# Performance work log

Measured on AMD Instinct MI355X. Metric: run time of the kernel, lower is better.

The kernel has to match this reference:

```python
import jax, jax.numpy as jnp
import numpy as np

EMB = 128
WIN = 5
OUT = 128
VOCAB = 50257
PAD_IDX = 0


def setup_inputs() -> dict:
    key = jax.random.key(0)
    k1, k2, k3 = jax.random.split(key, 3)
    x = jax.random.randint(k1, (16, 2048), 0, VOCAB, dtype=jnp.int64 if jax.config.jax_enable_x64 else jnp.int32)
    emb_table = jax.random.normal(k2, (VOCAB, EMB), dtype=jnp.float32)
    emb_table = emb_table.at[PAD_IDX].set(0.0)  # padding_idx row is zero
    fan_in = EMB * WIN
    bound = 1.0 / np.sqrt(fan_in)
    kw, kb = jax.random.split(k3)
    W = jax.random.uniform(kw, (OUT, fan_in), minval=-bound, maxval=bound, dtype=jnp.float32)
    b = jax.random.uniform(kb, (OUT,), minval=-bound, maxval=bound, dtype=jnp.float32)
    return {"x": x, "emb_table": emb_table, "W": W, "b": b}


def reference(x, emb_table, W, b):
    B, S = x.shape
    no_pads = (WIN - 1) // 2
    emb = emb_table[x]                                   # (B, S, EMB) gather
    padded = jnp.pad(emb, ((0, 0), (no_pads, no_pads), (0, 0)))
    windows = jnp.stack([padded[:, k:k + S] for k in range(WIN)], axis=2)
    flat = windows.reshape(B, S, WIN * EMB)
    y = jnp.einsum('bsk,ok->bso', flat, W) + b           # (B, S, OUT)
    return jax.nn.gelu(y, approximate=False)             # torch GELU default is exact
```

## Files before the change

### kernel.cpp

```cpp
#include <hip/hip_runtime.h>
#include <hip/hip_bf16.h>


#define EMB   128
#define WIN   5
#define OUTC  128
#define SEQ   2048
#define KTOT  640
#define MTILE 64
#define NTILE 64

#define EMB_STRIDE 136
#define SW_STRIDE  136

typedef __bf16  bf16x8 __attribute__((ext_vector_type(8)));
typedef float   f32x4  __attribute__((ext_vector_type(4)));
typedef ushort  u16x8  __attribute__((ext_vector_type(8)));

__device__ inline ushort f2bf(float f) {
    __bf16 h = (__bf16)f;
    return __builtin_bit_cast(ushort, h);
}

__device__ inline u16x8 cvt8v(float4 v0, float4 v1) {
    u16x8 o;
    o[0] = f2bf(v0.x); o[1] = f2bf(v0.y); o[2] = f2bf(v0.z); o[3] = f2bf(v0.w);
    o[4] = f2bf(v1.x); o[5] = f2bf(v1.y); o[6] = f2bf(v1.z); o[7] = f2bf(v1.w);
    return o;
}

__global__ __launch_bounds__(256, 4) void conv_encoder_kernel(
    const int* __restrict__ x,
    const float* __restrict__ emb,
    const float* __restrict__ W,
    const float* __restrict__ bias,
    float* __restrict__ out)
{
    __shared__ ushort sEmb[(MTILE + WIN - 1) * EMB_STRIDE];
    __shared__ ushort sW[NTILE * SW_STRIDE];

    const int tid = threadIdx.x;
    const int mi  = blockIdx.x;
    const int n0  = blockIdx.y * NTILE;
    const int m0  = mi * MTILE;
    const int bb  = m0 >> 11;
    const int s0  = m0 & (SEQ - 1);

    float4 preA[4], preB[4];
    #pragma unroll
    for (int t = 0; t < 4; ++t) {
        const int idx = tid + t * 256;
        const int r = idx >> 4, c = idx & 15;
        const float* p = W + (size_t)(n0 + r) * KTOT + c * 8;
        preA[t] = *(const float4*)p;
        preB[t] = *(const float4*)(p + 4);
    }

    {
        const int xbase = bb * SEQ;
        for (int idx = tid; idx < (MTILE + WIN - 1) * 16; idx += 256) {
            const int r = idx >> 4, c = idx & 15;
            const int s = s0 - 2 + r;
            const int tok = (s >= 0 && s < SEQ) ? x[xbase + s] : 0;
            const float* p = emb + (size_t)tok * EMB + c * 8;
            *(u16x8*)(&sEmb[r * EMB_STRIDE + c * 8]) =
                cvt8v(*(const float4*)p, *(const float4*)(p + 4));
        }
    }

    const int lane = tid & 63;
    const int wv   = tid >> 6;
    const int qr   = (wv >> 1) * 32;
    const int qc   = (wv & 1) * 32;
    const int lr   = lane & 15;
    const int lk8  = (lane >> 4) * 8;

    f32x4 acc[2][2];
    #pragma unroll
    for (int i = 0; i < 2; ++i)
        #pragma unroll
        for (int j = 0; j < 2; ++j)
            acc[i][j] = (f32x4){0.f, 0.f, 0.f, 0.f};

    for (int win = 0; win < WIN; ++win) {
        __syncthreads();
        #pragma unroll
        for (int t = 0; t < 4; ++t) {
            const int idx = tid + t * 256;
            const int r = idx >> 4, c = idx & 15;
            *(u16x8*)(&sW[r * SW_STRIDE + c * 8]) = cvt8v(preA[t], preB[t]);
        }
        __syncthreads();

        if (win + 1 < WIN) {
            #pragma unroll
            for (int t = 0; t < 4; ++t) {
                const int idx = tid + t * 256;
                const int r = idx >> 4, c = idx & 15;
                const float* p = W + (size_t)(n0 + r) * KTOT + (win + 1) * EMB + c * 8;
                preA[t] = *(const float4*)p;
                preB[t] = *(const float4*)(p + 4);
            }
        }

        #pragma unroll
        for (int kc = 0; kc < 4; ++kc) {
            const int e = kc * 32 + lk8;
            bf16x8 afr[2], bfr[2];
            #pragma unroll
            for (int i = 0; i < 2; ++i)
                afr[i] = *(const bf16x8*)(&sEmb[(qr + i * 16 + lr + win) * EMB_STRIDE + e]);
            #pragma unroll
            for (int j = 0; j < 2; ++j)
                bfr[j] = *(const bf16x8*)(&sW[(qc + j * 16 + lr) * SW_STRIDE + e]);
            #pragma unroll
            for (int i = 0; i < 2; ++i)
                #pragma unroll
                for (int j = 0; j < 2; ++j)
                    acc[i][j] = __builtin_amdgcn_mfma_f32_16x16x32_bf16(afr[i], bfr[j], acc[i][j], 0, 0, 0);
        }
    }

    float bj[2];
    #pragma unroll
    for (int j = 0; j < 2; ++j)
        bj[j] = bias[n0 + qc + j * 16 + lr];

    const int rbase = (lane >> 4) * 4;
    #pragma unroll
    for (int i = 0; i < 2; ++i) {
        #pragma unroll
        for (int j = 0; j < 2; ++j) {
            const int col = n0 + qc + j * 16 + lr;
            #pragma unroll
            for (int r = 0; r < 4; ++r) {
                const int row = m0 + qr + i * 16 + rbase + r;
                const float y = acc[i][j][r] + bj[j];
                const float g = 0.5f * y * (1.0f + erff(y * 0.70710678118654752f));
                out[(size_t)row * OUTC + col] = g;
            }
        }
    }
}

extern "C" void kernel_launch(void* const* d_in, const int* in_sizes, int n_in,
                              void* d_out, int out_size, void* d_ws, size_t ws_size,
                              hipStream_t stream) {
    (void)in_sizes; (void)n_in; (void)d_ws; (void)ws_size; (void)out_size;
    const int* x        = (const int*)d_in[0];
    const float* emb    = (const float*)d_in[1];
    const float* Wm     = (const float*)d_in[2];
    const float* bias   = (const float*)d_in[3];
    float* out          = (float*)d_out;

    dim3 grid(32768 / MTILE, OUTC / NTILE);
    dim3 block(256);
    hipLaunchKernelGGL(conv_encoder_kernel, grid, block, 0, stream, x, emb, Wm, bias, out);
}
```

Measured before the change: 93.29 us.

## Pre-convert gathered embeddings and weights to bf16 in a separate prep kernel

```diff
diff --git a/kernel.cpp b/kernel.cpp
--- a/kernel.cpp
+++ b/kernel.cpp
@@ -11,7 +11,16 @@
 #define NTILE 64
 
 #define EMB_STRIDE 136
-#define SW_STRIDE  136
+
+#define ABF_OFF   0
+#define ABF_BYTES (32768ull * 128 * 2)
+#define WBF_OFF   ABF_BYTES
+#define WBF_BYTES (128ull * 640 * 2)
+#define ZROW_OFF  (WBF_OFF + WBF_BYTES)
+#define NTASK_A   (32768 * 16)
+#define NTASK_W   (10240)
+#define NTASK_Z   (16)
+#define NTASK_TOT (NTASK_A + NTASK_W + NTASK_Z)
 
 typedef __bf16  bf16x8 __attribute__((ext_vector_type(8)));
 typedef float   f32x4  __attribute__((ext_vector_type(4)));
@@ -29,15 +38,38 @@
     return o;
 }
 
-__global__ __launch_bounds__(256, 4) void conv_encoder_kernel(
+__global__ __launch_bounds__(256) void prep_kernel(
     const int* __restrict__ x,
     const float* __restrict__ emb,
     const float* __restrict__ W,
+    ushort* __restrict__ ws)
+{
+    int t = blockIdx.x * 256 + threadIdx.x;
+    for (; t < NTASK_TOT; t += gridDim.x * 256) {
+        if (t < NTASK_A) {
+            const int row = t >> 4, c = t & 15;
+            const int tok = x[row];
+            const float* p = emb + (size_t)tok * EMB + c * 8;
+            *(u16x8*)(ws + (size_t)row * EMB + c * 8) =
+                cvt8v(*(const float4*)p, *(const float4*)(p + 4));
+        } else if (t < NTASK_A + NTASK_W) {
+            const int i = t - NTASK_A;
+            const float* p = W + (size_t)i * 8;
+            *(u16x8*)(ws + WBF_OFF / 2 + (size_t)i * 8) =
+                cvt8v(*(const float4*)p, *(const float4*)(p + 4));
+        } else {
+            const int i = t - NTASK_A - NTASK_W;
+            *(u16x8*)(ws + ZROW_OFF / 2 + (size_t)i * 8) = (u16x8){0,0,0,0,0,0,0,0};
+        }
+    }
+}
+
+__global__ __launch_bounds__(256, 4) void conv_encoder_kernel(
+    const ushort* __restrict__ ws,
     const float* __restrict__ bias,
     float* __restrict__ out)
 {
     __shared__ ushort sEmb[(MTILE + WIN - 1) * EMB_STRIDE];
-    __shared__ ushort sW[NTILE * SW_STRIDE];
 
     const int tid = threadIdx.x;
     const int mi  = blockIdx.x;
@@ -46,27 +78,19 @@
     const int bb  = m0 >> 11;
     const int s0  = m0 & (SEQ - 1);
 
-    float4 preA[4], preB[4];
-    #pragma unroll
-    for (int t = 0; t < 4; ++t) {
-        const int idx = tid + t * 256;
+    const ushort* Abf  = ws;
+    const ushort* Wbf  = ws + WBF_OFF / 2;
+    const ushort* zrow = ws + ZROW_OFF / 2;
+
+    for (int idx = tid; idx < (MTILE + WIN - 1) * 16; idx += 256) {
         const int r = idx >> 4, c = idx & 15;
-        const float* p = W + (size_t)(n0 + r) * KTOT + c * 8;
-        preA[t] = *(const float4*)p;
-        preB[t] = *(const float4*)(p + 4);
+        const int s = s0 - 2 + r;
+        const ushort* src = (s >= 0 && s < SEQ)
+            ? Abf + ((size_t)(bb * SEQ + s)) * EMB + c * 8
+            : zrow + c * 8;
+        *(u16x8*)(&sEmb[r * EMB_STRIDE + c * 8]) = *(const u16x8*)src;
     }
-
-    {
-        const int xbase = bb * SEQ;
-        for (int idx = tid; idx < (MTILE + WIN - 1) * 16; idx += 256) {
-            const int r = idx >> 4, c = idx & 15;
-            const int s = s0 - 2 + r;
-            const int tok = (s >= 0 && s < SEQ) ? x[xbase + s] : 0;
-            const float* p = emb + (size_t)tok * EMB + c * 8;
-            *(u16x8*)(&sEmb[r * EMB_STRIDE + c * 8]) =
-                cvt8v(*(const float4*)p, *(const float4*)(p + 4));
-        }
-    }
+    __syncthreads();
 
     const int lane = tid & 63;
     const int wv   = tid >> 6;
@@ -82,37 +106,20 @@
         for (int j = 0; j < 2; ++j)
             acc[i][j] = (f32x4){0.f, 0.f, 0.f, 0.f};
 
+    const ushort* wbase0 = Wbf + (size_t)(n0 + qc + lr) * KTOT + lk8;
+    const ushort* wbase1 = wbase0 + 16 * KTOT;
+
     for (int win = 0; win < WIN; ++win) {
-        __syncthreads();
-        #pragma unroll
-        for (int t = 0; t < 4; ++t) {
-            const int idx = tid + t * 256;
-            const int r = idx >> 4, c = idx & 15;
-            *(u16x8*)(&sW[r * SW_STRIDE + c * 8]) = cvt8v(preA[t], preB[t]);
-        }
-        __syncthreads();
-
-        if (win + 1 < WIN) {
-            #pragma unroll
-            for (int t = 0; t < 4; ++t) {
-                const int idx = tid + t * 256;
-                const int r = idx >> 4, c = idx & 15;
-                const float* p = W + (size_t)(n0 + r) * KTOT + (win + 1) * EMB + c * 8;
-                preA[t] = *(const float4*)p;
-                preB[t] = *(const float4*)(p + 4);
-            }
-        }
-
         #pragma unroll
         for (int kc = 0; kc < 4; ++kc) {
-            const int e = kc * 32 + lk8;
+            const int e  = kc * 32 + lk8;
+            const int ko = win * EMB + kc * 32;
             bf16x8 afr[2], bfr[2];
+            bfr[0] = *(const bf16x8*)(wbase0 + ko);
+            bfr[1] = *(const bf16x8*)(wbase1 + ko);
             #pragma unroll
             for (int i = 0; i < 2; ++i)
                 afr[i] = *(const bf16x8*)(&sEmb[(qr + i * 16 + lr + win) * EMB_STRIDE + e]);
-            #pragma unroll
-            for (int j = 0; j < 2; ++j)
-                bfr[j] = *(const bf16x8*)(&sW[(qc + j * 16 + lr) * SW_STRIDE + e]);
             #pragma unroll
             for (int i = 0; i < 2; ++i)
                 #pragma unroll
@@ -146,14 +153,15 @@
 extern "C" void kernel_launch(void* const* d_in, const int* in_sizes, int n_in,
                               void* d_out, int out_size, void* d_ws, size_t ws_size,
                               hipStream_t stream) {
-    (void)in_sizes; (void)n_in; (void)d_ws; (void)ws_size; (void)out_size;
+    (void)in_sizes; (void)n_in; (void)ws_size; (void)out_size;
     const int* x        = (const int*)d_in[0];
     const float* emb    = (const float*)d_in[1];
     const float* Wm     = (const float*)d_in[2];
     const float* bias   = (const float*)d_in[3];
     float* out          = (float*)d_out;
+    ushort* ws          = (ushort*)d_ws;
 
-    dim3 grid(32768 / MTILE, OUTC / NTILE);
-    dim3 block(256);
-    hipLaunchKernelGGL(conv_encoder_kernel, grid, block, 0, stream, x, emb, Wm, bias, out);
+    hipLaunchKernelGGL(prep_kernel, dim3(2048), dim3(256), 0, stream, x, emb, Wm, ws);
+    hipLaunchKernelGGL(conv_encoder_kernel, dim3(32768 / MTILE, OUTC / NTILE), dim3(256),
+                       0, stream, ws, bias, out);
 }
```

Result: slower. 106.9 us (+14.6%).

## Compute full output width per block and read weights directly into registers

Applied to the files above, without the earlier changes.

```diff
diff --git a/kernel.cpp b/kernel.cpp
--- a/kernel.cpp
+++ b/kernel.cpp
@@ -8,10 +8,8 @@
 #define SEQ   2048
 #define KTOT  640
 #define MTILE 64
-#define NTILE 64
 
 #define EMB_STRIDE 136
-#define SW_STRIDE  136
 
 typedef __bf16  bf16x8 __attribute__((ext_vector_type(8)));
 typedef float   f32x4  __attribute__((ext_vector_type(4)));
@@ -37,24 +35,11 @@
     float* __restrict__ out)
 {
     __shared__ ushort sEmb[(MTILE + WIN - 1) * EMB_STRIDE];
-    __shared__ ushort sW[NTILE * SW_STRIDE];
 
     const int tid = threadIdx.x;
-    const int mi  = blockIdx.x;
-    const int n0  = blockIdx.y * NTILE;
-    const int m0  = mi * MTILE;
+    const int m0  = blockIdx.x * MTILE;
     const int bb  = m0 >> 11;
     const int s0  = m0 & (SEQ - 1);
-
-    float4 preA[4], preB[4];
-    #pragma unroll
-    for (int t = 0; t < 4; ++t) {
-        const int idx = tid + t * 256;
-        const int r = idx >> 4, c = idx & 15;
-        const float* p = W + (size_t)(n0 + r) * KTOT + c * 8;
-        preA[t] = *(const float4*)p;
-        preB[t] = *(const float4*)(p + 4);
-    }
 
     {
         const int xbase = bb * SEQ;
@@ -67,54 +52,39 @@
                 cvt8v(*(const float4*)p, *(const float4*)(p + 4));
         }
     }
+    __syncthreads();
 
     const int lane = tid & 63;
     const int wv   = tid >> 6;
-    const int qr   = (wv >> 1) * 32;
-    const int qc   = (wv & 1) * 32;
     const int lr   = lane & 15;
     const int lk8  = (lane >> 4) * 8;
 
-    f32x4 acc[2][2];
+    f32x4 acc[4][2];
     #pragma unroll
-    for (int i = 0; i < 2; ++i)
+    for (int i = 0; i < 4; ++i)
         #pragma unroll
         for (int j = 0; j < 2; ++j)
             acc[i][j] = (f32x4){0.f, 0.f, 0.f, 0.f};
 
+    const float* w0 = W + (size_t)(wv * 32 + lr) * KTOT + lk8;
+    const float* w1 = w0 + 16 * KTOT;
+
+    #pragma unroll
     for (int win = 0; win < WIN; ++win) {
-        __syncthreads();
-        #pragma unroll
-        for (int t = 0; t < 4; ++t) {
-            const int idx = tid + t * 256;
-            const int r = idx >> 4, c = idx & 15;
-            *(u16x8*)(&sW[r * SW_STRIDE + c * 8]) = cvt8v(preA[t], preB[t]);
-        }
-        __syncthreads();
-
-        if (win + 1 < WIN) {
-            #pragma unroll
-            for (int t = 0; t < 4; ++t) {
-                const int idx = tid + t * 256;
-                const int r = idx >> 4, c = idx & 15;
-                const float* p = W + (size_t)(n0 + r) * KTOT + (win + 1) * EMB + c * 8;
-                preA[t] = *(const float4*)p;
-                preB[t] = *(const float4*)(p + 4);
-            }
-        }
-
         #pragma unroll
         for (int kc = 0; kc < 4; ++kc) {
-            const int e = kc * 32 + lk8;
-            bf16x8 afr[2], bfr[2];
+            const int e  = kc * 32 + lk8;
+            const int ko = win * EMB + kc * 32;
+            bf16x8 bfr[2], afr[4];
+            bfr[0] = __builtin_bit_cast(bf16x8,
+                cvt8v(*(const float4*)(w0 + ko), *(const float4*)(w0 + ko + 4)));
+            bfr[1] = __builtin_bit_cast(bf16x8,
+                cvt8v(*(const float4*)(w1 + ko), *(const float4*)(w1 + ko + 4)));
             #pragma unroll
-            for (int i = 0; i < 2; ++i)
-                afr[i] = *(const bf16x8*)(&sEmb[(qr + i * 16 + lr + win) * EMB_STRIDE + e]);
+            for (int i = 0; i < 4; ++i)
+                afr[i] = *(const bf16x8*)(&sEmb[(i * 16 + lr + win) * EMB_STRIDE + e]);
             #pragma unroll
-            for (int j = 0; j < 2; ++j)
-                bfr[j] = *(const bf16x8*)(&sW[(qc + j * 16 + lr) * SW_STRIDE + e]);
-            #pragma unroll
-            for (int i = 0; i < 2; ++i)
+            for (int i = 0; i < 4; ++i)
                 #pragma unroll
                 for (int j = 0; j < 2; ++j)
                     acc[i][j] = __builtin_amdgcn_mfma_f32_16x16x32_bf16(afr[i], bfr[j], acc[i][j], 0, 0, 0);
@@ -124,17 +94,17 @@
     float bj[2];
     #pragma unroll
     for (int j = 0; j < 2; ++j)
-        bj[j] = bias[n0 + qc + j * 16 + lr];
+        bj[j] = bias[wv * 32 + j * 16 + lr];
 
     const int rbase = (lane >> 4) * 4;
     #pragma unroll
-    for (int i = 0; i < 2; ++i) {
+    for (int i = 0; i < 4; ++i) {
         #pragma unroll
         for (int j = 0; j < 2; ++j) {
-            const int col = n0 + qc + j * 16 + lr;
+            const int col = wv * 32 + j * 16 + lr;
             #pragma unroll
             for (int r = 0; r < 4; ++r) {
-                const int row = m0 + qr + i * 16 + rbase + r;
+                const int row = m0 + i * 16 + rbase + r;
                 const float y = acc[i][j][r] + bj[j];
                 const float g = 0.5f * y * (1.0f + erff(y * 0.70710678118654752f));
                 out[(size_t)row * OUTC + col] = g;
@@ -153,7 +123,7 @@
     const float* bias   = (const float*)d_in[3];
     float* out          = (float*)d_out;
 
-    dim3 grid(32768 / MTILE, OUTC / NTILE);
+    dim3 grid(32768 / MTILE);
     dim3 block(256);
     hipLaunchKernelGGL(conv_encoder_kernel, grid, block, 0, stream, x, emb, Wm, bias, out);
 }
```

New measurement: 103.2 us. 10.6% more time.
